# Optimization experiments

Hardware: AMD Instinct MI355X
Metric: run time of the kernel (lower is better)

Reference implementation:

```python
import jax, jax.numpy as jnp
import numpy as np

NUM_AREAS = 4
NUM_TICKS = 4
AREA_N = 2048          # neurons per area
N = NUM_AREAS * AREA_N # total neurons = 8192
D_IN = 1024
N_CLASSES = 1024
BATCH = 512
THRESHOLD = 0.05


def setup_inputs() -> dict:
    key = jax.random.key(0)
    ks = jax.random.split(key, 9)
    x = jax.random.normal(ks[0], (BATCH, D_IN), jnp.float32)
    Rw = jax.random.normal(ks[1], (NUM_AREAS, AREA_N, D_IN), jnp.float32) * 0.02
    rb = jax.random.normal(ks[2], (NUM_AREAS, AREA_N), jnp.float32) * 0.02
    W_blocks = jax.random.normal(ks[3], (NUM_AREAS, NUM_AREAS, AREA_N, AREA_N), jnp.float32) * 0.02
    # bias only on diagonal blocks (in_area == out_area), else zeros, as in torch code
    b_full = jax.random.normal(ks[4], (NUM_AREAS, AREA_N), jnp.float32) * 0.02
    b_blocks = jnp.zeros((NUM_AREAS, NUM_AREAS, AREA_N), jnp.float32)
    b_blocks = b_blocks.at[jnp.arange(NUM_AREAS), jnp.arange(NUM_AREAS)].set(b_full)
    # mask init: 0.5 on diagonal blocks, 0.05 off-diagonal
    eye = jnp.eye(NUM_AREAS, dtype=jnp.float32)
    mask = (0.05 + 0.45 * eye)[:, :, None, None] * jnp.ones((NUM_AREAS, NUM_AREAS, AREA_N, AREA_N), jnp.float32)
    Ow = jax.random.normal(ks[5], (N_CLASSES, N), jnp.float32) * 0.02
    Ob = jax.random.normal(ks[6], (N_CLASSES,), jnp.float32) * 0.02
    # KMeans-like neuron partition: random permutation split into equal areas
    area_idx = jax.random.permutation(ks[7], N).reshape(NUM_AREAS, AREA_N).astype(jnp.int64)
    return {"x": x, "Rw": Rw, "rb": rb, "W_blocks": W_blocks, "b_blocks": b_blocks,
            "mask": mask, "Ow": Ow, "Ob": Ob, "area_idx": area_idx}


def reference(x, Rw, rb, W_blocks, b_blocks, mask, Ow, Ob, area_idx):
    # Initial per-area encoding: Z[a] = tanh(x @ Rw[a].T + rb[a]) -> [A, B, n]
    Z = jnp.tanh(jnp.einsum('bd,and->abn', x, Rw) + rb[:, None, :])
    history = [Z]
    # Effective masked weights (clamp mask to [0,1])
    Weff = W_blocks * jnp.clip(mask, 0.0, 1.0)  # [A_out, A_in, n_out, n_in]
    for _ in range(NUM_TICKS):
        # data-dependent skip: connection fires only if mean|Z_in| > threshold
        gate = (jnp.mean(jnp.abs(Z), axis=(1, 2)) > THRESHOLD).astype(Z.dtype)  # [A_in]
        Zg = Z * gate[:, None, None]
        Z_next = jnp.einsum('ibm,oinm->obn', Zg, Weff)
        Z_next = Z_next + jnp.einsum('i,oin->on', gate, b_blocks)[:, None, :]
        Z = jnp.tanh(Z_next)
        history.append(Z)
    B = x.shape[0]
    # Scatter per-area activations back to flat neuron order
    Zperm = jnp.transpose(Z, (1, 0, 2)).reshape(B, N)  # columns ordered as area_idx.reshape(-1)
    Z_flat = jnp.zeros((B, N), x.dtype).at[:, area_idx.reshape(-1)].set(Zperm)
    logits = Z_flat @ Ow.T + Ob
    return logits, jnp.stack(history)  # history: [T+1, A, B, n]
```

## Files before the change

kernel.cpp:

```cpp
#include <hip/hip_runtime.h>
#include <stdint.h>

typedef unsigned short u16;
typedef float floatx4 __attribute__((ext_vector_type(4)));
typedef __bf16 bf16x8 __attribute__((ext_vector_type(8)));

#define NUM_AREAS 4
#define AN 2048
#define NTOT 8192
#define BATCH 512
#define DIN 1024
#define NCLS 1024
#define THRESHOLD 0.05f
#define BAN (BATCH * AN)

__device__ __forceinline__ u16 f2bf(float f) {
    union { float f; unsigned u; } v; v.f = f;
    unsigned r = v.u + 0x7fffu + ((v.u >> 16) & 1u);
    return (u16)(r >> 16);
}

__device__ __forceinline__ void load_lds16(const u16* g, u16* l) {
    __builtin_amdgcn_global_load_lds((const __attribute__((address_space(1))) void*)g,
                                     (__attribute__((address_space(3))) void*)l,
                                     16, 0, 0);
}

__device__ __forceinline__ void gemm_tiles(const u16* __restrict__ A, int lda,
                                           const u16* __restrict__ Bm, int ldb,
                                           int klen, u16* smemA, u16* smemB,
                                           floatx4 acc[4][4]) {
    const int tid = threadIdx.x;
    const int t8 = tid * 8;
    const int lane = tid & 63;
    const int quad = lane >> 4;
    const int l15 = lane & 15;
    const int wm = ((tid >> 7) & 1) * 64;
    const int wn = ((tid >> 6) & 1) * 64;
    for (int k0 = 0; k0 < klen; k0 += 32) {
        __syncthreads();
#pragma unroll
        for (int q = 0; q < 2; ++q) {
            const int flat = q * 2048 + t8;
            const int r = flat >> 5;
            const int kk = flat & 31;
            load_lds16(A + (size_t)r * lda + (k0 + kk), smemA + flat);
            load_lds16(Bm + (size_t)r * ldb + (k0 + kk), smemB + flat);
        }
        __syncthreads();
        bf16x8 av[4], bv[4];
#pragma unroll
        for (int i = 0; i < 4; ++i)
            av[i] = *(const bf16x8*)(smemA + (wm + i * 16 + l15) * 32 + quad * 8);
#pragma unroll
        for (int i = 0; i < 4; ++i)
            bv[i] = *(const bf16x8*)(smemB + (wn + i * 16 + l15) * 32 + quad * 8);
#pragma unroll
        for (int mt = 0; mt < 4; ++mt)
#pragma unroll
            for (int nt = 0; nt < 4; ++nt)
                acc[mt][nt] = __builtin_amdgcn_mfma_f32_16x16x32_bf16(av[mt], bv[nt], acc[mt][nt], 0, 0, 0);
    }
}

__global__ void k_init(const float* __restrict__ Ob, float* __restrict__ out,
                       float* __restrict__ gacc) {
    const int i = blockIdx.x * 256 + threadIdx.x;
    if (i < BATCH * NCLS) out[i] = Ob[i & (NCLS - 1)];
    if (i < 32) gacc[i] = 0.f;
}

__global__ void k_cvt(const float* __restrict__ src, u16* __restrict__ dst, int n8) {
    const int i = blockIdx.x * 256 + threadIdx.x;
    if (i >= n8) return;
    const float4 x0 = ((const float4*)src)[2 * i];
    const float4 x1 = ((const float4*)src)[2 * i + 1];
    uint4 o;
    o.x = (unsigned)f2bf(x0.x) | ((unsigned)f2bf(x0.y) << 16);
    o.y = (unsigned)f2bf(x0.z) | ((unsigned)f2bf(x0.w) << 16);
    o.z = (unsigned)f2bf(x1.x) | ((unsigned)f2bf(x1.y) << 16);
    o.w = (unsigned)f2bf(x1.z) | ((unsigned)f2bf(x1.w) << 16);
    ((uint4*)dst)[i] = o;
}

__global__ void k_weff(const float* __restrict__ W, const float* __restrict__ mask,
                       u16* __restrict__ dst, int n8) {
    const int i = blockIdx.x * 256 + threadIdx.x;
    if (i >= n8) return;
    const float4 w0 = ((const float4*)W)[2 * i];
    const float4 w1 = ((const float4*)W)[2 * i + 1];
    const float4 m0 = ((const float4*)mask)[2 * i];
    const float4 m1 = ((const float4*)mask)[2 * i + 1];
    #define CL(m) fminf(fmaxf((m), 0.f), 1.f)
    uint4 o;
    o.x = (unsigned)f2bf(w0.x * CL(m0.x)) | ((unsigned)f2bf(w0.y * CL(m0.y)) << 16);
    o.y = (unsigned)f2bf(w0.z * CL(m0.z)) | ((unsigned)f2bf(w0.w * CL(m0.w)) << 16);
    o.z = (unsigned)f2bf(w1.x * CL(m1.x)) | ((unsigned)f2bf(w1.y * CL(m1.y)) << 16);
    o.w = (unsigned)f2bf(w1.z * CL(m1.z)) | ((unsigned)f2bf(w1.w * CL(m1.w)) << 16);
    #undef CL
    ((uint4*)dst)[i] = o;
}

__global__ void k_enc(const u16* __restrict__ xbf, const u16* __restrict__ rwbf,
                      const float* __restrict__ rb, float* __restrict__ hist0,
                      u16* __restrict__ z0, float* __restrict__ gacc) {
    __shared__ __align__(16) u16 smemA[4096];
    __shared__ __align__(16) u16 smemB[4096];
    __shared__ float red[4];
    floatx4 acc[4][4] = {};
    const int mb = blockIdx.y, nb = blockIdx.x;
    gemm_tiles(xbf + (size_t)mb * 128 * DIN, DIN,
               rwbf + (size_t)nb * 128 * DIN, DIN, DIN, smemA, smemB, acc);
    const int tid = threadIdx.x, lane = tid & 63, quad = lane >> 4, l15 = lane & 15;
    const int wm = ((tid >> 7) & 1) * 64, wn = ((tid >> 6) & 1) * 64;
    const int cbase = nb * 128;
    const int area = cbase >> 11;
    float asum = 0.f;
#pragma unroll
    for (int nt = 0; nt < 4; ++nt) {
        const int col = cbase + wn + nt * 16 + l15;
        const int n = col & (AN - 1);
        const float bias = rb[col];
#pragma unroll
        for (int mt = 0; mt < 4; ++mt) {
#pragma unroll
            for (int r = 0; r < 4; ++r) {
                const int row = mb * 128 + wm + mt * 16 + quad * 4 + r;
                const float z = tanhf(acc[mt][nt][r] + bias);
                asum += fabsf(z);
                const size_t idx = (size_t)area * BAN + (size_t)row * AN + n;
                hist0[idx] = z;
                z0[idx] = f2bf(z);
            }
        }
    }
    for (int off = 32; off > 0; off >>= 1) asum += __shfl_down(asum, off, 64);
    if (lane == 0) red[tid >> 6] = asum;
    __syncthreads();
    if (tid == 0) atomicAdd(&gacc[area], red[0] + red[1] + red[2] + red[3]);
}

__global__ void k_tick(const u16* __restrict__ zprev, const u16* __restrict__ weff,
                       const float* __restrict__ bblk, const float* __restrict__ gin,
                       float* __restrict__ hist, u16* __restrict__ zcur,
                       float* __restrict__ gout) {
    __shared__ __align__(16) u16 smemA[4096];
    __shared__ __align__(16) u16 smemB[4096];
    __shared__ float red[4];
    floatx4 acc[4][4] = {};
    const int mb = blockIdx.y, nb = blockIdx.x;
    const int cbase = nb * 128;
    const int o = cbase >> 11;
    const int nbase = cbase & (AN - 1);
    const float thr = THRESHOLD * (float)BAN;
    bool gg[4];
#pragma unroll
    for (int i = 0; i < 4; ++i) gg[i] = gin[i] > thr;
#pragma unroll
    for (int i = 0; i < 4; ++i) {
        if (!gg[i]) continue;
        gemm_tiles(zprev + (size_t)i * BAN + (size_t)mb * 128 * AN, AN,
                   weff + ((size_t)(o * 4 + i) * AN + nbase) * AN, AN, AN,
                   smemA, smemB, acc);
    }
    const int tid = threadIdx.x, lane = tid & 63, quad = lane >> 4, l15 = lane & 15;
    const int wm = ((tid >> 7) & 1) * 64, wn = ((tid >> 6) & 1) * 64;
    float asum = 0.f;
#pragma unroll
    for (int nt = 0; nt < 4; ++nt) {
        const int n = nbase + wn + nt * 16 + l15;
        float bias = 0.f;
#pragma unroll
        for (int i = 0; i < 4; ++i)
            if (gg[i]) bias += bblk[(o * 4 + i) * AN + n];
#pragma unroll
        for (int mt = 0; mt < 4; ++mt) {
#pragma unroll
            for (int r = 0; r < 4; ++r) {
                const int row = mb * 128 + wm + mt * 16 + quad * 4 + r;
                const float z = tanhf(acc[mt][nt][r] + bias);
                asum += fabsf(z);
                const size_t idx = (size_t)o * BAN + (size_t)row * AN + n;
                hist[idx] = z;
                zcur[idx] = f2bf(z);
            }
        }
    }
    for (int off = 32; off > 0; off >>= 1) asum += __shfl_down(asum, off, 64);
    if (lane == 0) red[tid >> 6] = asum;
    __syncthreads();
    if (tid == 0) atomicAdd(&gout[o], red[0] + red[1] + red[2] + red[3]);
}

__global__ void k_scatter(const u16* __restrict__ z4, const int* __restrict__ aidx,
                          u16* __restrict__ zflat) {
    const int i = blockIdx.x * 256 + threadIdx.x;
    const int n = i & (AN - 1);
    const int bb = (i >> 11) & (BATCH - 1);
    const int a = i >> 20;
    const int j = aidx[a * AN + n];
    zflat[(size_t)bb * NTOT + j] = z4[i];
}

__global__ void k_out(const u16* __restrict__ zflat, const u16* __restrict__ owbf,
                      float* __restrict__ out) {
    __shared__ __align__(16) u16 smemA[4096];
    __shared__ __align__(16) u16 smemB[4096];
    floatx4 acc[4][4] = {};
    const int nb = blockIdx.x, mb = blockIdx.y, ks = blockIdx.z;
    gemm_tiles(zflat + (size_t)mb * 128 * NTOT + ks * 2048, NTOT,
               owbf + (size_t)nb * 128 * NTOT + ks * 2048, NTOT, 2048,
               smemA, smemB, acc);
    const int tid = threadIdx.x, lane = tid & 63, quad = lane >> 4, l15 = lane & 15;
    const int wm = ((tid >> 7) & 1) * 64, wn = ((tid >> 6) & 1) * 64;
#pragma unroll
    for (int mt = 0; mt < 4; ++mt)
#pragma unroll
        for (int nt = 0; nt < 4; ++nt)
#pragma unroll
            for (int r = 0; r < 4; ++r) {
                const int row = mb * 128 + wm + mt * 16 + quad * 4 + r;
                const int col = nb * 128 + wn + nt * 16 + l15;
                atomicAdd(&out[(size_t)row * NCLS + col], acc[mt][nt][r]);
            }
}

extern "C" void kernel_launch(void* const* d_in, const int* in_sizes, int n_in,
                              void* d_out, int out_size, void* d_ws, size_t ws_size,
                              hipStream_t stream) {
    (void)in_sizes; (void)n_in; (void)out_size; (void)ws_size;
    const float* x    = (const float*)d_in[0];
    const float* Rw   = (const float*)d_in[1];
    const float* rb   = (const float*)d_in[2];
    const float* Wb   = (const float*)d_in[3];
    const float* bblk = (const float*)d_in[4];
    const float* mask = (const float*)d_in[5];
    const float* Ow   = (const float*)d_in[6];
    const float* Ob   = (const float*)d_in[7];
    const int*   aidx = (const int*)d_in[8];

    float* out  = (float*)d_out;
    float* hist = out + (size_t)BATCH * NCLS;

    char* ws = (char*)d_ws;
    size_t off = 0;
    auto alloc = [&](size_t bytes) -> char* {
        char* p = ws + off;
        off += (bytes + 255) & ~(size_t)255;
        return p;
    };
    u16* weffbf = (u16*)alloc((size_t)16 * AN * AN * 2);
    u16* rwbf   = (u16*)alloc((size_t)NTOT * DIN * 2);
    u16* xbf    = (u16*)alloc((size_t)BATCH * DIN * 2);
    u16* owbf   = (u16*)alloc((size_t)NCLS * NTOT * 2);
    u16* zb0    = (u16*)alloc((size_t)NUM_AREAS * BAN * 2);
    u16* zb1    = (u16*)alloc((size_t)NUM_AREAS * BAN * 2);
    u16* zflat  = (u16*)alloc((size_t)BATCH * NTOT * 2);
    float* gacc = (float*)alloc(32 * 4);
    u16* zb[2]  = { zb0, zb1 };

    k_init<<<(BATCH * NCLS + 255) / 256, 256, 0, stream>>>(Ob, out, gacc);
    k_cvt<<<(BATCH * DIN / 8) / 256, 256, 0, stream>>>(x, xbf, BATCH * DIN / 8);
    k_cvt<<<(NTOT * DIN / 8) / 256, 256, 0, stream>>>(Rw, rwbf, NTOT * DIN / 8);
    k_cvt<<<(NCLS * NTOT / 8) / 256, 256, 0, stream>>>(Ow, owbf, NCLS * NTOT / 8);
    k_weff<<<(16 * AN * AN / 8) / 256, 256, 0, stream>>>(Wb, mask, weffbf, 16 * AN * AN / 8);

    dim3 g1(64, 4);
    k_enc<<<g1, 256, 0, stream>>>(xbf, rwbf, rb, hist, zb[0], gacc);
    for (int t = 1; t <= 4; ++t) {
        k_tick<<<g1, 256, 0, stream>>>(zb[(t + 1) & 1], weffbf, bblk,
                                       gacc + (t - 1) * 4,
                                       hist + (size_t)t * NUM_AREAS * BAN,
                                       zb[t & 1], gacc + t * 4);
    }
    k_scatter<<<(NUM_AREAS * BAN) / 256, 256, 0, stream>>>(zb[0], aidx, zflat);
    k_out<<<dim3(8, 4, 4), 256, 0, stream>>>(zflat, owbf, out);
}
```

Measured before the change: 1.225 ms.

## Split tick GEMM over input areas with separate reduction epilogue kernel

Each tick's GEMM grid gains a third dimension over the four input areas, so each block computes one area's partial product and writes FP32 partials to a workspace. A new epilogue kernel sums the gated partials, adds the bias, applies tanh and writes history and bf16 activations with vectorized stores. The intent is to raise the block count from 256 to 1024 for better occupancy across CUs, at the cost of roughly 64MB of extra FP32 partial traffic per tick. Workspace buffers for the Rw/Ow conversions and zflat are aliased into the partial buffer, and the Ow conversion is moved after the ticks.

```diff
diff --git a/kernel.cpp b/kernel.cpp
--- a/kernel.cpp
+++ b/kernel.cpp
@@ -140,54 +140,76 @@
     if (tid == 0) atomicAdd(&gacc[area], red[0] + red[1] + red[2] + red[3]);
 }
 
-__global__ void k_tick(const u16* __restrict__ zprev, const u16* __restrict__ weff,
-                       const float* __restrict__ bblk, const float* __restrict__ gin,
-                       float* __restrict__ hist, u16* __restrict__ zcur,
-                       float* __restrict__ gout) {
+__global__ void k_tick_mm(const u16* __restrict__ zprev, const u16* __restrict__ weff,
+                          const float* __restrict__ gin, float* __restrict__ zacc) {
     __shared__ __align__(16) u16 smemA[4096];
     __shared__ __align__(16) u16 smemB[4096];
-    __shared__ float red[4];
+    const int nb = blockIdx.x, mb = blockIdx.y, i = blockIdx.z;
+    const float thr = THRESHOLD * (float)BAN;
+    if (!(gin[i] > thr)) return;
     floatx4 acc[4][4] = {};
-    const int mb = blockIdx.y, nb = blockIdx.x;
     const int cbase = nb * 128;
     const int o = cbase >> 11;
     const int nbase = cbase & (AN - 1);
-    const float thr = THRESHOLD * (float)BAN;
-    bool gg[4];
-#pragma unroll
-    for (int i = 0; i < 4; ++i) gg[i] = gin[i] > thr;
-#pragma unroll
-    for (int i = 0; i < 4; ++i) {
-        if (!gg[i]) continue;
-        gemm_tiles(zprev + (size_t)i * BAN + (size_t)mb * 128 * AN, AN,
-                   weff + ((size_t)(o * 4 + i) * AN + nbase) * AN, AN, AN,
-                   smemA, smemB, acc);
-    }
+    gemm_tiles(zprev + (size_t)i * BAN + (size_t)mb * 128 * AN, AN,
+               weff + ((size_t)(o * 4 + i) * AN + nbase) * AN, AN, AN,
+               smemA, smemB, acc);
+    float* __restrict__ dst = zacc + ((size_t)i * 4 + o) * BAN;
     const int tid = threadIdx.x, lane = tid & 63, quad = lane >> 4, l15 = lane & 15;
     const int wm = ((tid >> 7) & 1) * 64, wn = ((tid >> 6) & 1) * 64;
-    float asum = 0.f;
 #pragma unroll
     for (int nt = 0; nt < 4; ++nt) {
         const int n = nbase + wn + nt * 16 + l15;
-        float bias = 0.f;
-#pragma unroll
-        for (int i = 0; i < 4; ++i)
-            if (gg[i]) bias += bblk[(o * 4 + i) * AN + n];
 #pragma unroll
         for (int mt = 0; mt < 4; ++mt) {
 #pragma unroll
             for (int r = 0; r < 4; ++r) {
                 const int row = mb * 128 + wm + mt * 16 + quad * 4 + r;
-                const float z = tanhf(acc[mt][nt][r] + bias);
-                asum += fabsf(z);
-                const size_t idx = (size_t)o * BAN + (size_t)row * AN + n;
-                hist[idx] = z;
-                zcur[idx] = f2bf(z);
+                dst[(size_t)row * AN + n] = acc[mt][nt][r];
             }
         }
     }
+}
+
+__global__ void k_tick_ep(const float* __restrict__ zacc, const float* __restrict__ bblk,
+                          const float* __restrict__ gin, float* __restrict__ hist,
+                          u16* __restrict__ zcur, float* __restrict__ gout) {
+    __shared__ float red[4];
+    const int tid = threadIdx.x;
+    const int t8 = (blockIdx.x * 256 + tid) * 8;
+    const int o = t8 >> 20;
+    const int n = t8 & (AN - 1);
+    const int io = t8 & (BAN - 1);
+    const float thr = THRESHOLD * (float)BAN;
+    float s[8] = {0.f, 0.f, 0.f, 0.f, 0.f, 0.f, 0.f, 0.f};
+#pragma unroll
+    for (int i = 0; i < 4; ++i) {
+        if (!(gin[i] > thr)) continue;
+        const float4* p = (const float4*)(zacc + ((size_t)i * 4 + o) * BAN + io);
+        const float4 x0 = p[0], x1 = p[1];
+        const float4* bb = (const float4*)(bblk + (size_t)(o * 4 + i) * AN + n);
+        const float4 b0 = bb[0], b1 = bb[1];
+        s[0] += x0.x + b0.x; s[1] += x0.y + b0.y; s[2] += x0.z + b0.z; s[3] += x0.w + b0.w;
+        s[4] += x1.x + b1.x; s[5] += x1.y + b1.y; s[6] += x1.z + b1.z; s[7] += x1.w + b1.w;
+    }
+    float asum = 0.f;
+    float4 h0, h1;
+    uint4 zb;
+    float z0 = tanhf(s[0]), z1 = tanhf(s[1]), z2 = tanhf(s[2]), z3 = tanhf(s[3]);
+    float z4 = tanhf(s[4]), z5 = tanhf(s[5]), z6 = tanhf(s[6]), z7 = tanhf(s[7]);
+    asum = fabsf(z0) + fabsf(z1) + fabsf(z2) + fabsf(z3)
+         + fabsf(z4) + fabsf(z5) + fabsf(z6) + fabsf(z7);
+    h0.x = z0; h0.y = z1; h0.z = z2; h0.w = z3;
+    h1.x = z4; h1.y = z5; h1.z = z6; h1.w = z7;
+    zb.x = (unsigned)f2bf(z0) | ((unsigned)f2bf(z1) << 16);
+    zb.y = (unsigned)f2bf(z2) | ((unsigned)f2bf(z3) << 16);
+    zb.z = (unsigned)f2bf(z4) | ((unsigned)f2bf(z5) << 16);
+    zb.w = (unsigned)f2bf(z6) | ((unsigned)f2bf(z7) << 16);
+    ((float4*)(hist + t8))[0] = h0;
+    ((float4*)(hist + t8))[1] = h1;
+    *((uint4*)(zcur + t8)) = zb;
     for (int off = 32; off > 0; off >>= 1) asum += __shfl_down(asum, off, 64);
-    if (lane == 0) red[tid >> 6] = asum;
+    if ((tid & 63) == 0) red[tid >> 6] = asum;
     __syncthreads();
     if (tid == 0) atomicAdd(&gout[o], red[0] + red[1] + red[2] + red[3]);
 }
@@ -250,29 +272,32 @@
         return p;
     };
     u16* weffbf = (u16*)alloc((size_t)16 * AN * AN * 2);
-    u16* rwbf   = (u16*)alloc((size_t)NTOT * DIN * 2);
+    float* zacc = (float*)alloc((size_t)16 * BAN * 4);
+    u16* rwbf  = (u16*)zacc;
+    u16* owbf  = (u16*)((char*)zacc + ((size_t)16 << 20));
+    u16* zflat = (u16*)((char*)zacc + ((size_t)32 << 20));
     u16* xbf    = (u16*)alloc((size_t)BATCH * DIN * 2);
-    u16* owbf   = (u16*)alloc((size_t)NCLS * NTOT * 2);
     u16* zb0    = (u16*)alloc((size_t)NUM_AREAS * BAN * 2);
     u16* zb1    = (u16*)alloc((size_t)NUM_AREAS * BAN * 2);
-    u16* zflat  = (u16*)alloc((size_t)BATCH * NTOT * 2);
     float* gacc = (float*)alloc(32 * 4);
     u16* zb[2]  = { zb0, zb1 };
 
     k_init<<<(BATCH * NCLS + 255) / 256, 256, 0, stream>>>(Ob, out, gacc);
     k_cvt<<<(BATCH * DIN / 8) / 256, 256, 0, stream>>>(x, xbf, BATCH * DIN / 8);
     k_cvt<<<(NTOT * DIN / 8) / 256, 256, 0, stream>>>(Rw, rwbf, NTOT * DIN / 8);
-    k_cvt<<<(NCLS * NTOT / 8) / 256, 256, 0, stream>>>(Ow, owbf, NCLS * NTOT / 8);
     k_weff<<<(16 * AN * AN / 8) / 256, 256, 0, stream>>>(Wb, mask, weffbf, 16 * AN * AN / 8);
 
     dim3 g1(64, 4);
     k_enc<<<g1, 256, 0, stream>>>(xbf, rwbf, rb, hist, zb[0], gacc);
+    dim3 gmm(64, 4, 4);
     for (int t = 1; t <= 4; ++t) {
-        k_tick<<<g1, 256, 0, stream>>>(zb[(t + 1) & 1], weffbf, bblk,
-                                       gacc + (t - 1) * 4,
-                                       hist + (size_t)t * NUM_AREAS * BAN,
-                                       zb[t & 1], gacc + t * 4);
-    }
+        k_tick_mm<<<gmm, 256, 0, stream>>>(zb[(t + 1) & 1], weffbf,
+                                           gacc + (t - 1) * 4, zacc);
+        k_tick_ep<<<2048, 256, 0, stream>>>(zacc, bblk, gacc + (t - 1) * 4,
+                                            hist + (size_t)t * NUM_AREAS * BAN,
+                                            zb[t & 1], gacc + t * 4);
+    }
+    k_cvt<<<(NCLS * NTOT / 8) / 256, 256, 0, stream>>>(Ow, owbf, NCLS * NTOT / 8);
     k_scatter<<<(NUM_AREAS * BAN) / 256, 256, 0, stream>>>(zb[0], aidx, zflat);
     k_out<<<dim3(8, 4, 4), 256, 0, stream>>>(zflat, owbf, out);
 }
```

Result: faster. 1.126 ms (-8.1%).
